# Performance work log

Measured on AMD Instinct MI355X. Metric: run time of the kernel, lower is better.

Reference implementation:

```python
import jax, jax.numpy as jnp
import numpy as np

B, T, E = 2, 2048, 768
H = 12
HD = E // H          # 64
ROT = 32             # rotary dim (= head_dim // 2 in CLVP)
SCALE = HD ** -0.5


def rotate_half(x):
    # split last dim into (2, d/2), rotate second half by 90 deg
    x = x.reshape(*x.shape[:-1], 2, x.shape[-1] // 2)
    x1, x2 = x[..., 0, :], x[..., 1, :]
    return jnp.concatenate([-x2, x1], axis=-1)


def apply_rotary_pos_emb(state, freqs):
    # state: (B*H, T, HD); freqs: (1, T, ROT)
    pos_emb_len = freqs.shape[-1]
    s_l, s_r = state[..., :pos_emb_len], state[..., pos_emb_len:]
    f = freqs[:, :, -s_l.shape[-1]:]
    s_l = s_l * jnp.cos(f) + rotate_half(s_l) * jnp.sin(f)
    return jnp.concatenate([s_l, s_r], axis=-1)


def setup_inputs() -> dict:
    key = jax.random.key(0)
    ks = jax.random.split(key, 6)
    hidden_states = jax.random.normal(ks[0], (B, T, E), dtype=jnp.float32)
    rotary_pos_emb = jax.random.uniform(ks[1], (1, T, ROT), dtype=jnp.float32)
    Wq = jax.random.normal(ks[2], (E, E), dtype=jnp.float32) * 0.02
    Wk = jax.random.normal(ks[3], (E, E), dtype=jnp.float32) * 0.02
    Wv = jax.random.normal(ks[4], (E, E), dtype=jnp.float32) * 0.02
    Wo = jax.random.normal(ks[5], (E, E), dtype=jnp.float32) * 0.02
    bo = jnp.zeros((E,), dtype=jnp.float32)
    return {"hidden_states": hidden_states, "rotary_pos_emb": rotary_pos_emb,
            "Wq": Wq, "Wk": Wk, "Wv": Wv, "Wo": Wo, "bo": bo}


def _shape(x):
    # (B, T, E) -> (B*H, T, HD)
    return x.reshape(B, T, H, HD).transpose(0, 2, 1, 3).reshape(B * H, T, HD)


def reference(hidden_states, rotary_pos_emb, Wq, Wk, Wv, Wo, bo):
    # nn.Linear: x @ W.T
    q = _shape(hidden_states @ Wq.T * SCALE)
    k = _shape(hidden_states @ Wk.T)
    v = _shape(hidden_states @ Wv.T)

    q = apply_rotary_pos_emb(q, rotary_pos_emb)
    k = apply_rotary_pos_emb(k, rotary_pos_emb)
    v = apply_rotary_pos_emb(v, rotary_pos_emb)  # CLVP applies RoPE to V too

    attn = jax.nn.softmax(jnp.einsum('bqd,bkd->bqk', q, k), axis=-1)  # (B*H, T, T)
    out = jnp.einsum('bqk,bkd->bqd', attn, v)                          # (B*H, T, HD)
    out = out.reshape(B, H, T, HD).transpose(0, 2, 1, 3).reshape(B, T, E)
    return out @ Wo.T + bo
```

## Files before the change

### kernel.cpp

```cpp
#include <hip/hip_runtime.h>
#include <hip/hip_bf16.h>

typedef unsigned short ushort_t;
typedef __attribute__((ext_vector_type(8))) short short8;
typedef __attribute__((ext_vector_type(4))) float f32x4;

constexpr int B  = 2;
constexpr int T  = 2048;
constexpr int E  = 768;
constexpr int H  = 12;
constexpr int HD = 64;

__device__ __forceinline__ ushort_t f2bf(float x) {
  unsigned int u = __float_as_uint(x);
  u += 0x7fffu + ((u >> 16) & 1u);
  return (ushort_t)(u >> 16);
}

__device__ __forceinline__ unsigned int pack_bf2(float a, float b) {
  __hip_bfloat162 h = __float22bfloat162_rn(float2{a, b});
  return *(unsigned int*)&h;
}

__device__ __forceinline__ int swz(int row, int col) {
  return row * 64 + ((((col >> 3) ^ (row & 7)) << 3) | (col & 7));
}

__global__ __launch_bounds__(256) void cvt_all(
    const float* __restrict__ X,  const float* __restrict__ Wq,
    const float* __restrict__ Wk, const float* __restrict__ Wv,
    const float* __restrict__ Wo, const float* __restrict__ rope,
    ushort_t* __restrict__ Xb,  ushort_t* __restrict__ Wqb,
    ushort_t* __restrict__ Wkb, ushort_t* __restrict__ Wvb,
    ushort_t* __restrict__ Wob, float* __restrict__ ct, float* __restrict__ st)
{
  constexpr int NX4 = (B * T * E) / 4;
  constexpr int NW4 = (E * E) / 4;
  constexpr int NC4 = NX4 + 4 * NW4;
  int i = blockIdx.x * 256 + threadIdx.x;
  if (i < NC4) {
    const float* s; ushort_t* d; int j;
    if (i < NX4) { s = X; d = Xb; j = i; }
    else {
      int t = i - NX4;
      int w = t / NW4; j = t - w * NW4;
      s = (w == 0) ? Wq : (w == 1) ? Wk : (w == 2) ? Wv : Wo;
      d = (w == 0) ? Wqb : (w == 1) ? Wkb : (w == 2) ? Wvb : Wob;
    }
    float4 v = ((const float4*)s)[j];
    ushort4 o;
    o.x = f2bf(v.x); o.y = f2bf(v.y); o.z = f2bf(v.z); o.w = f2bf(v.w);
    ((ushort4*)d)[j] = o;
  } else {
    int j = (i - NC4) * 4;
    float4 f = *(const float4*)(rope + j);
    float c, s;
    sincosf(f.x, &s, &c); ct[j+0] = c; st[j+0] = s;
    sincosf(f.y, &s, &c); ct[j+1] = c; st[j+1] = s;
    sincosf(f.z, &s, &c); ct[j+2] = c; st[j+2] = s;
    sincosf(f.w, &s, &c); ct[j+3] = c; st[j+3] = s;
  }
}

__global__ __launch_bounds__(256) void qkv_gemm(
    const ushort_t* __restrict__ Xb,
    const ushort_t* __restrict__ Wqb, const ushort_t* __restrict__ Wkb,
    const ushort_t* __restrict__ Wvb,
    const float* __restrict__ ct, const float* __restrict__ st,
    ushort_t* __restrict__ qfb, ushort_t* __restrict__ kfb, ushort_t* __restrict__ vfb)
{
  __shared__ __align__(16) ushort_t smem[128 * 64 + 64 * 64];
  ushort_t* Xs = smem;
  ushort_t* Ws = smem + 128 * 64;
  const int tid  = threadIdx.x;
  const int wave = tid >> 6;
  const int lane = tid & 63;
  const int l15  = lane & 15, quad = lane >> 4;
  const int n0 = blockIdx.x * 64;
  const int m0 = blockIdx.y * 128;
  const int z  = blockIdx.z;
  const ushort_t* Wt = (z == 0) ? Wqb : (z == 1) ? Wkb : Wvb;
  const int h = n0 >> 6;

  f32x4 acc[2][4];
  #pragma unroll
  for (int i = 0; i < 2; ++i)
    #pragma unroll
    for (int j = 0; j < 4; ++j) acc[i][j] = (f32x4){0.f, 0.f, 0.f, 0.f};

  const int srX = tid >> 1, scX = (tid & 1) * 32;
  const int srW = tid >> 2, scW = (tid & 3) * 16;

  for (int k0 = 0; k0 < E; k0 += 64) {
    uint4 x0 = *(const uint4*)(Xb + (size_t)(m0 + srX) * E + k0 + scX);
    uint4 x1 = *(const uint4*)(Xb + (size_t)(m0 + srX) * E + k0 + scX + 8);
    uint4 x2 = *(const uint4*)(Xb + (size_t)(m0 + srX) * E + k0 + scX + 16);
    uint4 x3 = *(const uint4*)(Xb + (size_t)(m0 + srX) * E + k0 + scX + 24);
    uint4 w0 = *(const uint4*)(Wt + (size_t)(n0 + srW) * E + k0 + scW);
    uint4 w1 = *(const uint4*)(Wt + (size_t)(n0 + srW) * E + k0 + scW + 8);
    *(uint4*)&Xs[swz(srX, scX)]      = x0;
    *(uint4*)&Xs[swz(srX, scX + 8)]  = x1;
    *(uint4*)&Xs[swz(srX, scX + 16)] = x2;
    *(uint4*)&Xs[swz(srX, scX + 24)] = x3;
    *(uint4*)&Ws[swz(srW, scW)]      = w0;
    *(uint4*)&Ws[swz(srW, scW + 8)]  = w1;
    __syncthreads();
    short8 a[2][2];
    #pragma unroll
    for (int mt = 0; mt < 2; ++mt)
      #pragma unroll
      for (int kh = 0; kh < 2; ++kh)
        a[mt][kh] = *(const short8*)&Xs[swz(wave * 32 + mt * 16 + l15, kh * 32 + quad * 8)];
    #pragma unroll
    for (int nt = 0; nt < 4; ++nt) {
      #pragma unroll
      for (int kh = 0; kh < 2; ++kh) {
        short8 bb = *(const short8*)&Ws[swz(nt * 16 + l15, kh * 32 + quad * 8)];
        #pragma unroll
        for (int mt = 0; mt < 2; ++mt)
          acc[mt][nt] = __builtin_amdgcn_mfma_f32_16x16x32_bf16(a[mt][kh], bb, acc[mt][nt], 0, 0, 0);
      }
    }
    __syncthreads();
  }

  const int b  = m0 >> 11;
  const int t0 = m0 & (T - 1);
  const int bh = b * H + h;
  const float qscale = (z == 0) ? 0.125f : 1.0f;

  if (z < 2) {
    #pragma unroll
    for (int mt = 0; mt < 2; ++mt) {
      #pragma unroll
      for (int r = 0; r < 4; ++r) {
        int mloc = wave * 32 + mt * 16 + quad * 4 + r;
        int t = (m0 + mloc) & (T - 1);
        float s0 = acc[mt][0][r] * qscale;
        float s1 = acc[mt][1][r] * qscale;
        float c0v = ct[t * 32 + l15],      sn0 = st[t * 32 + l15];
        float c1v = ct[t * 32 + 16 + l15], sn1 = st[t * 32 + 16 + l15];
        smem[swz(mloc, l15)]      = f2bf(s0 * c0v - s1 * sn0);
        smem[swz(mloc, 16 + l15)] = f2bf(s1 * c1v + s0 * sn1);
        smem[swz(mloc, 32 + l15)] = f2bf(acc[mt][2][r] * qscale);
        smem[swz(mloc, 48 + l15)] = f2bf(acc[mt][3][r] * qscale);
      }
    }
    __syncthreads();
    if (z == 0) {
      #pragma unroll
      for (int i = 0; i < 4; ++i) {
        int p = tid + 256 * i;
        int qtl = p >> 7, kh = (p >> 6) & 1, ln = p & 63;
        int tl = qtl * 16 + (ln & 15);
        int d  = kh * 32 + (ln >> 4) * 8;
        uint4 v = *(const uint4*)&smem[swz(tl, d)];
        size_t off = ((size_t)((bh * 128 + (t0 >> 4) + qtl) * 2 + kh)) * 512 + ln * 8;
        *(uint4*)(qfb + off) = v;
      }
    } else {
      #pragma unroll
      for (int i = 0; i < 4; ++i) {
        int p = tid + 256 * i;
        int ktl = p >> 9, mt = (p >> 7) & 3, kh = (p >> 6) & 1, ln = p & 63;
        int tl = ktl * 64 + mt * 16 + (ln & 15);
        int d  = kh * 32 + (ln >> 4) * 8;
        uint4 v = *(const uint4*)&smem[swz(tl, d)];
        size_t off = ((size_t)(((bh * 32 + (t0 >> 6) + ktl) * 4 + mt) * 2 + kh)) * 512 + ln * 8;
        *(uint4*)(kfb + off) = v;
      }
    }
  } else {
    #pragma unroll
    for (int mt = 0; mt < 2; ++mt) {
      #pragma unroll
      for (int r = 0; r < 4; ++r) {
        int mloc = wave * 32 + mt * 16 + quad * 4 + r;
        int t = (m0 + mloc) & (T - 1);
        float s0 = acc[mt][0][r], s1 = acc[mt][1][r];
        float c0v = ct[t * 32 + l15],      sn0 = st[t * 32 + l15];
        float c1v = ct[t * 32 + 16 + l15], sn1 = st[t * 32 + 16 + l15];
        smem[(l15)      * 132 + mloc] = f2bf(s0 * c0v - s1 * sn0);
        smem[(16 + l15) * 132 + mloc] = f2bf(s1 * c1v + s0 * sn1);
        smem[(32 + l15) * 132 + mloc] = f2bf(acc[mt][2][r]);
        smem[(48 + l15) * 132 + mloc] = f2bf(acc[mt][3][r]);
      }
    }
    __syncthreads();
    #pragma unroll
    for (int i = 0; i < 4; ++i) {
      int p = tid + 256 * i;
      int ktl = p >> 9, nt = (p >> 7) & 3, kh = (p >> 6) & 1, ln = p & 63;
      int d  = nt * 16 + (ln & 15);
      int tl = ktl * 64 + kh * 32 + (ln >> 4) * 8;
      uint4 v = *(const uint4*)&smem[d * 132 + tl];
      size_t off = ((size_t)(((bh * 32 + (t0 >> 6) + ktl) * 4 + nt) * 2 + kh)) * 512 + ln * 8;
      *(uint4*)(vfb + off) = v;
    }
  }
}

__global__ __launch_bounds__(256) void attn_kernel(
    const ushort_t* __restrict__ qfb, const ushort_t* __restrict__ kfb,
    const ushort_t* __restrict__ vfb, ushort_t* __restrict__ cbuf)
{
  __shared__ __align__(16) ushort_t Ps[4][32 * 40];
  __shared__ __align__(16) float Osh[2][32][66];
  __shared__ float Lsh[2][32];
  const int tid  = threadIdx.x;
  const int wave = tid >> 6;
  const int wq = wave >> 1, wk = wave & 1;
  const int lane = tid & 63;
  const int l15  = lane & 15, quad = lane >> 4;
  const int q0 = blockIdx.x * 64;
  const int bh = blockIdx.y;
  const ushort_t* Qf = qfb + (size_t)bh * (T * HD);
  const ushort_t* Kf = kfb + (size_t)bh * (T * HD);
  const ushort_t* Vf = vfb + (size_t)bh * (T * HD);
  ushort_t* Pw = &Ps[wave][0];

  short8 qa[2][2];
  #pragma unroll
  for (int qg = 0; qg < 2; ++qg)
    #pragma unroll
    for (int kh = 0; kh < 2; ++kh)
      qa[qg][kh] = *(const short8*)(Qf + ((size_t)(((q0 >> 4) + wq * 2 + qg) * 2 + kh)) * 512 + lane * 8);

  short8 ka[2][2], va[4];
  #pragma unroll
  for (int i = 0; i < 2; ++i)
    #pragma unroll
    for (int kh = 0; kh < 2; ++kh)
      ka[i][kh] = *(const short8*)(Kf + ((size_t)((wk * 2 + i) * 2 + kh)) * 512 + lane * 8);
  #pragma unroll
  for (int nt = 0; nt < 4; ++nt)
    va[nt] = *(const short8*)(Vf + ((size_t)(nt * 2 + wk)) * 512 + lane * 8);

  f32x4 o[2][4];
  #pragma unroll
  for (int qg = 0; qg < 2; ++qg)
    #pragma unroll
    for (int nt = 0; nt < 4; ++nt) o[qg][nt] = (f32x4){0.f, 0.f, 0.f, 0.f};
  float lsum[2] = {0.f, 0.f};

  for (int kt = 0; kt < T / 64; ++kt) {
    const int ktn = (kt + 1 < T / 64) ? kt + 1 : kt;
    short8 kn[2][2], vn[4];
    #pragma unroll
    for (int i = 0; i < 2; ++i)
      #pragma unroll
      for (int kh = 0; kh < 2; ++kh)
        kn[i][kh] = *(const short8*)(Kf + ((size_t)((ktn * 4 + wk * 2 + i) * 2 + kh)) * 512 + lane * 8);
    #pragma unroll
    for (int nt = 0; nt < 4; ++nt)
      vn[nt] = *(const short8*)(Vf + ((size_t)((ktn * 4 + nt) * 2 + wk)) * 512 + lane * 8);

    f32x4 ss[2][2];
    #pragma unroll
    for (int mt = 0; mt < 2; ++mt)
      #pragma unroll
      for (int qg = 0; qg < 2; ++qg) {
        ss[mt][qg] = (f32x4){0.f, 0.f, 0.f, 0.f};
        ss[mt][qg] = __builtin_amdgcn_mfma_f32_16x16x32_bf16(ka[mt][0], qa[qg][0], ss[mt][qg], 0, 0, 0);
        ss[mt][qg] = __builtin_amdgcn_mfma_f32_16x16x32_bf16(ka[mt][1], qa[qg][1], ss[mt][qg], 0, 0, 0);
      }

    #pragma unroll
    for (int qg = 0; qg < 2; ++qg) {
      #pragma unroll
      for (int mt = 0; mt < 2; ++mt) {
        float p0 = __expf(ss[mt][qg][0]);
        float p1 = __expf(ss[mt][qg][1]);
        float p2 = __expf(ss[mt][qg][2]);
        float p3 = __expf(ss[mt][qg][3]);
        lsum[qg] += (p0 + p1) + (p2 + p3);
        uint2 w2;
        w2.x = pack_bf2(p0, p1);
        w2.y = pack_bf2(p2, p3);
        *(uint2*)&Pw[(qg * 16 + l15) * 40 + mt * 16 + quad * 4] = w2;
      }
    }

    short8 pa0 = *(const short8*)&Pw[(l15) * 40 + quad * 8];
    short8 pa1 = *(const short8*)&Pw[(16 + l15) * 40 + quad * 8];
    #pragma unroll
    for (int nt = 0; nt < 4; ++nt) {
      o[0][nt] = __builtin_amdgcn_mfma_f32_16x16x32_bf16(pa0, va[nt], o[0][nt], 0, 0, 0);
      o[1][nt] = __builtin_amdgcn_mfma_f32_16x16x32_bf16(pa1, va[nt], o[1][nt], 0, 0, 0);
    }

    #pragma unroll
    for (int i = 0; i < 2; ++i) {
      ka[i][0] = kn[i][0];
      ka[i][1] = kn[i][1];
    }
    #pragma unroll
    for (int nt = 0; nt < 4; ++nt) va[nt] = vn[nt];
  }

  #pragma unroll
  for (int qg = 0; qg < 2; ++qg) {
    lsum[qg] += __shfl_xor(lsum[qg], 16);
    lsum[qg] += __shfl_xor(lsum[qg], 32);
  }

  if (wk == 0) {
    #pragma unroll
    for (int qg = 0; qg < 2; ++qg)
      #pragma unroll
      for (int nt = 0; nt < 4; ++nt)
        #pragma unroll
        for (int r = 0; r < 4; ++r)
          Osh[wq][qg * 16 + quad * 4 + r][nt * 16 + l15] = o[qg][nt][r];
    if (lane < 16) {
      Lsh[wq][l15]      = lsum[0];
      Lsh[wq][16 + l15] = lsum[1];
    }
  }
  __syncthreads();
  if (wk == 1) {
    const int b = bh / H, h = bh % H;
    #pragma unroll
    for (int qg = 0; qg < 2; ++qg) {
      float ltot = lsum[qg] + Lsh[wq][qg * 16 + l15];
      float inv0 = 1.0f / ltot;
      #pragma unroll
      for (int r = 0; r < 4; ++r) {
        float inv = __shfl(inv0, quad * 4 + r);
        int t = q0 + wq * 32 + qg * 16 + quad * 4 + r;
        size_t base = ((size_t)b * T + t) * E + h * HD;
        #pragma unroll
        for (int nt = 0; nt < 4; ++nt) {
          float v = o[qg][nt][r] + Osh[wq][qg * 16 + quad * 4 + r][nt * 16 + l15];
          cbuf[base + nt * 16 + l15] = f2bf(v * inv);
        }
      }
    }
  }
}

__global__ __launch_bounds__(256) void out_gemm(
    const ushort_t* __restrict__ Xc, const ushort_t* __restrict__ Wob,
    const float* __restrict__ bo, float* __restrict__ out)
{
  __shared__ __align__(16) ushort_t Xs[128 * 64];
  __shared__ __align__(16) ushort_t Ws[64 * 64];
  const int tid  = threadIdx.x;
  const int wave = tid >> 6;
  const int lane = tid & 63;
  const int l15  = lane & 15, quad = lane >> 4;
  const int n0 = blockIdx.x * 64;
  const int m0 = blockIdx.y * 128;

  f32x4 acc[2][4];
  #pragma unroll
  for (int i = 0; i < 2; ++i)
    #pragma unroll
    for (int j = 0; j < 4; ++j) acc[i][j] = (f32x4){0.f, 0.f, 0.f, 0.f};

  const int srX = tid >> 1, scX = (tid & 1) * 32;
  const int srW = tid >> 2, scW = (tid & 3) * 16;

  for (int k0 = 0; k0 < E; k0 += 64) {
    uint4 x0 = *(const uint4*)(Xc + (size_t)(m0 + srX) * E + k0 + scX);
    uint4 x1 = *(const uint4*)(Xc + (size_t)(m0 + srX) * E + k0 + scX + 8);
    uint4 x2 = *(const uint4*)(Xc + (size_t)(m0 + srX) * E + k0 + scX + 16);
    uint4 x3 = *(const uint4*)(Xc + (size_t)(m0 + srX) * E + k0 + scX + 24);
    uint4 w0 = *(const uint4*)(Wob + (size_t)(n0 + srW) * E + k0 + scW);
    uint4 w1 = *(const uint4*)(Wob + (size_t)(n0 + srW) * E + k0 + scW + 8);
    *(uint4*)&Xs[swz(srX, scX)]      = x0;
    *(uint4*)&Xs[swz(srX, scX + 8)]  = x1;
    *(uint4*)&Xs[swz(srX, scX + 16)] = x2;
    *(uint4*)&Xs[swz(srX, scX + 24)] = x3;
    *(uint4*)&Ws[swz(srW, scW)]      = w0;
    *(uint4*)&Ws[swz(srW, scW + 8)]  = w1;
    __syncthreads();
    short8 a[2][2];
    #pragma unroll
    for (int mt = 0; mt < 2; ++mt)
      #pragma unroll
      for (int kh = 0; kh < 2; ++kh)
        a[mt][kh] = *(const short8*)&Xs[swz(wave * 32 + mt * 16 + l15, kh * 32 + quad * 8)];
    #pragma unroll
    for (int nt = 0; nt < 4; ++nt) {
      #pragma unroll
      for (int kh = 0; kh < 2; ++kh) {
        short8 bb = *(const short8*)&Ws[swz(nt * 16 + l15, kh * 32 + quad * 8)];
        #pragma unroll
        for (int mt = 0; mt < 2; ++mt)
          acc[mt][nt] = __builtin_amdgcn_mfma_f32_16x16x32_bf16(a[mt][kh], bb, acc[mt][nt], 0, 0, 0);
      }
    }
    __syncthreads();
  }

  float bias[4];
  #pragma unroll
  for (int nt = 0; nt < 4; ++nt) bias[nt] = bo[n0 + nt * 16 + l15];
  #pragma unroll
  for (int mt = 0; mt < 2; ++mt) {
    #pragma unroll
    for (int r = 0; r < 4; ++r) {
      int m = m0 + wave * 32 + mt * 16 + quad * 4 + r;
      float* op = out + (size_t)m * E + n0;
      op[l15]      = acc[mt][0][r] + bias[0];
      op[16 + l15] = acc[mt][1][r] + bias[1];
      op[32 + l15] = acc[mt][2][r] + bias[2];
      op[48 + l15] = acc[mt][3][r] + bias[3];
    }
  }
}

extern "C" void kernel_launch(void* const* d_in, const int* in_sizes, int n_in,
                              void* d_out, int out_size, void* d_ws, size_t ws_size,
                              hipStream_t stream) {
  (void)in_sizes; (void)n_in; (void)out_size; (void)ws_size;
  const float* X    = (const float*)d_in[0];
  const float* rope = (const float*)d_in[1];
  const float* Wq   = (const float*)d_in[2];
  const float* Wk   = (const float*)d_in[3];
  const float* Wv   = (const float*)d_in[4];
  const float* Wo   = (const float*)d_in[5];
  const float* bo   = (const float*)d_in[6];
  float* out = (float*)d_out;

  const size_t NX = (size_t)B * T * E;
  const size_t NW = (size_t)E * E;
  const size_t NR = (size_t)T * 32;
  ushort_t* Xb  = (ushort_t*)d_ws;
  ushort_t* Wqb = Xb  + NX;
  ushort_t* Wkb = Wqb + NW;
  ushort_t* Wvb = Wkb + NW;
  ushort_t* Wob = Wvb + NW;
  ushort_t* qfb = Wob + NW;
  ushort_t* kfb = qfb + NX;
  ushort_t* vfb = kfb + NX;
  ushort_t* cb  = vfb + NX;
  float* ct = (float*)(cb + NX);
  float* st = ct + NR;

  const int total4 = (int)((NX + 4 * NW + NR) / 4);
  cvt_all<<<total4 / 256, 256, 0, stream>>>(X, Wq, Wk, Wv, Wo, rope,
                                            Xb, Wqb, Wkb, Wvb, Wob, ct, st);

  qkv_gemm<<<dim3(E / 64, (B * T) / 128, 3), 256, 0, stream>>>(
      Xb, Wqb, Wkb, Wvb, ct, st, qfb, kfb, vfb);
  attn_kernel<<<dim3(T / 64, B * H), 256, 0, stream>>>(qfb, kfb, vfb, cb);
  out_gemm<<<dim3(E / 64, (B * T) / 128), 256, 0, stream>>>(cb, Wob, bo, out);
}
```

Measured before the change: 166.2 us.

## Use direct global-to-LDS loads in GEMMs and exp2 softmax with folded log2e

Replaces the register-staged global loads and swizzled LDS stores in the QKV and output-projection GEMMs with global_load_lds 16-byte transfers. The swizzle is moved to the global address side so the LDS layout is unchanged. It also folds log2(e) into the query scale so the softmax can use exp2f instead of __expf. The direct loads cut VGPR use and instruction count, but correctness depends on the per-lane LDS placement matching the swizzled layout.

```diff
diff --git a/kernel.cpp b/kernel.cpp
--- a/kernel.cpp
+++ b/kernel.cpp
@@ -10,6 +10,7 @@
 constexpr int E  = 768;
 constexpr int H  = 12;
 constexpr int HD = 64;
+constexpr float QSCALE = 0.125f * 1.44269504088896f;
 
 __device__ __forceinline__ ushort_t f2bf(float x) {
   unsigned int u = __float_as_uint(x);
@@ -24,6 +25,12 @@
 
 __device__ __forceinline__ int swz(int row, int col) {
   return row * 64 + ((((col >> 3) ^ (row & 7)) << 3) | (col & 7));
+}
+
+__device__ __forceinline__ void gl_lds16(const ushort_t* g, ushort_t* l) {
+  __builtin_amdgcn_global_load_lds(
+      (const __attribute__((address_space(1))) unsigned int*)g,
+      (__attribute__((address_space(3))) unsigned int*)l, 16, 0, 0);
 }
 
 __global__ __launch_bounds__(256) void cvt_all(
@@ -88,22 +95,29 @@
     #pragma unroll
     for (int j = 0; j < 4; ++j) acc[i][j] = (f32x4){0.f, 0.f, 0.f, 0.f};
 
-  const int srX = tid >> 1, scX = (tid & 1) * 32;
-  const int srW = tid >> 2, scW = (tid & 3) * 16;
+  const int li8 = lane >> 3, lc8 = lane & 7;
+  const ushort_t* gX[4]; ushort_t* lX[4];
+  #pragma unroll
+  for (int j = 0; j < 4; ++j) {
+    int row = wave * 32 + j * 8 + li8;
+    int c = lc8 ^ (row & 7);
+    gX[j] = Xb + (size_t)(m0 + row) * E + c * 8;
+    lX[j] = Xs + (wave * 32 + j * 8) * 64;
+  }
+  const ushort_t* gW[2]; ushort_t* lW[2];
+  #pragma unroll
+  for (int j = 0; j < 2; ++j) {
+    int row = wave * 16 + j * 8 + li8;
+    int c = lc8 ^ (row & 7);
+    gW[j] = Wt + (size_t)(n0 + row) * E + c * 8;
+    lW[j] = Ws + (wave * 16 + j * 8) * 64;
+  }
 
   for (int k0 = 0; k0 < E; k0 += 64) {
-    uint4 x0 = *(const uint4*)(Xb + (size_t)(m0 + srX) * E + k0 + scX);
-    uint4 x1 = *(const uint4*)(Xb + (size_t)(m0 + srX) * E + k0 + scX + 8);
-    uint4 x2 = *(const uint4*)(Xb + (size_t)(m0 + srX) * E + k0 + scX + 16);
-    uint4 x3 = *(const uint4*)(Xb + (size_t)(m0 + srX) * E + k0 + scX + 24);
-    uint4 w0 = *(const uint4*)(Wt + (size_t)(n0 + srW) * E + k0 + scW);
-    uint4 w1 = *(const uint4*)(Wt + (size_t)(n0 + srW) * E + k0 + scW + 8);
-    *(uint4*)&Xs[swz(srX, scX)]      = x0;
-    *(uint4*)&Xs[swz(srX, scX + 8)]  = x1;
-    *(uint4*)&Xs[swz(srX, scX + 16)] = x2;
-    *(uint4*)&Xs[swz(srX, scX + 24)] = x3;
-    *(uint4*)&Ws[swz(srW, scW)]      = w0;
-    *(uint4*)&Ws[swz(srW, scW + 8)]  = w1;
+    #pragma unroll
+    for (int j = 0; j < 4; ++j) gl_lds16(gX[j] + k0, lX[j]);
+    #pragma unroll
+    for (int j = 0; j < 2; ++j) gl_lds16(gW[j] + k0, lW[j]);
     __syncthreads();
     short8 a[2][2];
     #pragma unroll
@@ -127,7 +141,7 @@
   const int b  = m0 >> 11;
   const int t0 = m0 & (T - 1);
   const int bh = b * H + h;
-  const float qscale = (z == 0) ? 0.125f : 1.0f;
+  const float qscale = (z == 0) ? QSCALE : 1.0f;
 
   if (z < 2) {
     #pragma unroll
@@ -269,10 +283,10 @@
     for (int qg = 0; qg < 2; ++qg) {
       #pragma unroll
       for (int mt = 0; mt < 2; ++mt) {
-        float p0 = __expf(ss[mt][qg][0]);
-        float p1 = __expf(ss[mt][qg][1]);
-        float p2 = __expf(ss[mt][qg][2]);
-        float p3 = __expf(ss[mt][qg][3]);
+        float p0 = exp2f(ss[mt][qg][0]);
+        float p1 = exp2f(ss[mt][qg][1]);
+        float p2 = exp2f(ss[mt][qg][2]);
+        float p3 = exp2f(ss[mt][qg][3]);
         lsum[qg] += (p0 + p1) + (p2 + p3);
         uint2 w2;
         w2.x = pack_bf2(p0, p1);
@@ -358,22 +372,29 @@
     #pragma unroll
     for (int j = 0; j < 4; ++j) acc[i][j] = (f32x4){0.f, 0.f, 0.f, 0.f};
 
-  const int srX = tid >> 1, scX = (tid & 1) * 32;
-  const int srW = tid >> 2, scW = (tid & 3) * 16;
+  const int li8 = lane >> 3, lc8 = lane & 7;
+  const ushort_t* gX[4]; ushort_t* lX[4];
+  #pragma unroll
+  for (int j = 0; j < 4; ++j) {
+    int row = wave * 32 + j * 8 + li8;
+    int c = lc8 ^ (row & 7);
+    gX[j] = Xc + (size_t)(m0 + row) * E + c * 8;
+    lX[j] = Xs + (wave * 32 + j * 8) * 64;
+  }
+  const ushort_t* gW[2]; ushort_t* lW[2];
+  #pragma unroll
+  for (int j = 0; j < 2; ++j) {
+    int row = wave * 16 + j * 8 + li8;
+    int c = lc8 ^ (row & 7);
+    gW[j] = Wob + (size_t)(n0 + row) * E + c * 8;
+    lW[j] = Ws + (wave * 16 + j * 8) * 64;
+  }
 
   for (int k0 = 0; k0 < E; k0 += 64) {
-    uint4 x0 = *(const uint4*)(Xc + (size_t)(m0 + srX) * E + k0 + scX);
-    uint4 x1 = *(const uint4*)(Xc + (size_t)(m0 + srX) * E + k0 + scX + 8);
-    uint4 x2 = *(const uint4*)(Xc + (size_t)(m0 + srX) * E + k0 + scX + 16);
-    uint4 x3 = *(const uint4*)(Xc + (size_t)(m0 + srX) * E + k0 + scX + 24);
-    uint4 w0 = *(const uint4*)(Wob + (size_t)(n0 + srW) * E + k0 + scW);
-    uint4 w1 = *(const uint4*)(Wob + (size_t)(n0 + srW) * E + k0 + scW + 8);
-    *(uint4*)&Xs[swz(srX, scX)]      = x0;
-    *(uint4*)&Xs[swz(srX, scX + 8)]  = x1;
-    *(uint4*)&Xs[swz(srX, scX + 16)] = x2;
-    *(uint4*)&Xs[swz(srX, scX + 24)] = x3;
-    *(uint4*)&Ws[swz(srW, scW)]      = w0;
-    *(uint4*)&Ws[swz(srW, scW + 8)]  = w1;
+    #pragma unroll
+    for (int j = 0; j < 4; ++j) gl_lds16(gX[j] + k0, lX[j]);
+    #pragma unroll
+    for (int j = 0; j < 2; ++j) gl_lds16(gW[j] + k0, lW[j]);
     __syncthreads();
     short8 a[2][2];
     #pragma unroll
```

Result: no change. 168.8 us (+1.6%).
